# Performance work log

Hardware: AMD Instinct MI355X
Metric: run time of the kernel (lower is better)

## Reference

```python
import jax, jax.numpy as jnp
import numpy as np

N = 50000        # nodes
E_RAND = 800000  # random edges; self-loops appended -> E = E_RAND + N
H = 4            # heads
D_IN = 256
D_HID = 64       # per-head hidden (H*D_HID == D_IN -> identity residual in layer 1)
D_OUT = 32       # classes per head
SLOPE = 0.2      # leaky-relu negative slope


def setup_inputs() -> dict:
    key = jax.random.key(0)
    ks = jax.random.split(key, 13)
    loops = jnp.arange(N, dtype=jnp.int32)
    src = jnp.concatenate([jax.random.randint(ks[0], (E_RAND,), 0, N, dtype=jnp.int32), loops])
    dst = jnp.concatenate([jax.random.randint(ks[1], (E_RAND,), 0, N, dtype=jnp.int32), loops])
    h = jax.random.normal(ks[2], (N, D_IN), dtype=jnp.float32)
    def w(k, shape, fan):
        return jax.random.normal(k, shape, dtype=jnp.float32) * (1.0 / np.sqrt(fan))
    return {
        "h": h, "src": src, "dst": dst,
        # layer 1 (tuple in_feats -> separate fc_src / fc_dst in dgl GATConv)
        "W1_src": w(ks[3], (D_IN, H * D_HID), D_IN),
        "W1_dst": w(ks[4], (D_IN, H * D_HID), D_IN),
        "al1": w(ks[5], (H, D_HID), D_HID),
        "ar1": w(ks[6], (H, D_HID), D_HID),
        # layer 2
        "W2_src": w(ks[7], (H * D_HID, H * D_OUT), H * D_HID),
        "W2_dst": w(ks[8], (H * D_HID, H * D_OUT), H * D_HID),
        "al2": w(ks[9], (H, D_OUT), D_OUT),
        "ar2": w(ks[10], (H, D_OUT), D_OUT),
        # residual projection for layer 2 (in_dim != heads*out)
        "Wres2": w(ks[11], (H * D_HID, H * D_OUT), H * D_HID),
    }


def gat_conv(h_node, src, dst, Ws, Wd, al, ar, heads, dout, resval):
    n = h_node.shape[0]
    fs = (h_node @ Ws).reshape(n, heads, dout)   # [N,H,D] projected src feats
    fd = (h_node @ Wd).reshape(n, heads, dout)
    el = jnp.sum(fs * al, axis=-1)               # [N,H]
    er = jnp.sum(fd * ar, axis=-1)               # [N,H]
    e = jax.nn.leaky_relu(el[src] + er[dst], SLOPE)           # [E,H] edge scores
    emax = jax.ops.segment_max(e, dst, num_segments=n)        # segment softmax over dst
    ex = jnp.exp(e - emax[dst])
    denom = jax.ops.segment_sum(ex, dst, num_segments=n)
    a = ex / denom[dst]                                        # [E,H] attention
    msg = fs[src] * a[:, :, None]                              # [E,H,D] gather * weight
    out = jax.ops.segment_sum(msg, dst, num_segments=n)       # [N,H,D] scatter-add
    return out + resval


def reference(h, src, dst, W1_src, W1_dst, al1, ar1, W2_src, W2_dst, al2, ar2, Wres2):
    # layer 1: identity residual (in_dim == heads*hidden), elu activation, flatten heads
    res1 = h.reshape(-1, H, D_HID)
    h1 = gat_conv(h, src, dst, W1_src, W1_dst, al1, ar1, H, D_HID, res1)
    h1 = jax.nn.elu(h1).reshape(-1, H * D_HID)
    # layer 2: linear residual, no activation, mean over heads
    res2 = (h1 @ Wres2).reshape(-1, H, D_OUT)
    h2 = gat_conv(h1, src, dst, W2_src, W2_dst, al2, ar2, H, D_OUT, res2)
    return h2.mean(axis=1)                                     # [N, num_classes]
```

## Files before the change

kernel.cpp:

```cpp
#include <hip/hip_runtime.h>
#include <hip/hip_bf16.h>

#define NN 50000
#define EE 850000
#define NBLK_SCAN 98

typedef unsigned short u16;
using short8 = __attribute__((ext_vector_type(8))) short;
using f32x4  = __attribute__((ext_vector_type(4))) float;

__device__ __forceinline__ float bf2f(u16 u) {
    union { unsigned int i; float f; } v; v.i = ((unsigned int)u) << 16; return v.f;
}
__device__ __forceinline__ u16 f2bf(float f) {
    __hip_bfloat16 h = __float2bfloat16(f);
    return *reinterpret_cast<u16*>(&h);
}

__device__ __forceinline__ float ld1(const void* X, size_t i, bool f32m) {
    return f32m ? ((const float*)X)[i] : bf2f(((const u16*)X)[i]);
}
__device__ __forceinline__ void load4(const void* X, size_t g, bool f32m, float o[4]) {
    if (f32m) {
        float4 v = ((const float4*)X)[g];
        o[0] = v.x; o[1] = v.y; o[2] = v.z; o[3] = v.w;
    } else {
        ushort4 v = ((const ushort4*)X)[g];
        o[0] = bf2f(v.x); o[1] = bf2f(v.y); o[2] = bf2f(v.z); o[3] = bf2f(v.w);
    }
}

__global__ void k_detect(const u16* __restrict__ hh, int* __restrict__ flag,
                         int* __restrict__ deg) {
    if (blockIdx.x != 0) {
        int i = (blockIdx.x - 1) * 256 + threadIdx.x;
        if (i < NN) deg[i] = 0;
        return;
    }
    __shared__ int sm[256];
    int t = threadIdx.x;
    int c = 0;
    for (int i = 0; i < 16; ++i) {
        u16 u = hh[t * 16 + i];
        int e = (u >> 7) & 0xFF;
        if (e != 0 && (e < 90 || e > 160)) ++c;
    }
    sm[t] = c;
    __syncthreads();
    for (int s = 128; s > 0; s >>= 1) {
        if (t < s) sm[t] += sm[t + s];
        __syncthreads();
    }
    if (t == 0) *flag = (sm[0] > 200) ? 1 : 0;
}

__global__ void k_prep(const void* __restrict__ W1s, const void* __restrict__ al1,
                       const void* __restrict__ W1d, const void* __restrict__ ar1,
                       const void* __restrict__ W2s, const void* __restrict__ al2,
                       const void* __restrict__ W2d, const void* __restrict__ ar2,
                       const void* __restrict__ Wres2, const int* __restrict__ dst,
                       u16* __restrict__ BT1, u16* __restrict__ BT2,
                       float* __restrict__ wl1, float* __restrict__ wr1,
                       float* __restrict__ wl2, float* __restrict__ wr2,
                       int* __restrict__ deg, const int* __restrict__ mode) {
    int bid = blockIdx.x;
    if (bid >= 528) {
        int e = (bid - 528) * 256 + threadIdx.x;
        if (e < EE) atomicAdd(&deg[dst[e]], 1);
        return;
    }
    bool f32m = (*mode) != 0;
    if (bid < 512) {
        int id = bid * 256 + threadIdx.x;
        int which = id >> 16;
        int rem = id & 65535;
        int n = rem >> 8, k = rem & 255;
        if (which == 0) {
            BT1[n * 256 + k] = f2bf(ld1(W1s, (size_t)k * 256 + n, f32m));
        } else {
            float v = (n < 128) ? ld1(W2s, (size_t)k * 128 + n, f32m)
                                : ld1(Wres2, (size_t)k * 128 + (n - 128), f32m);
            BT2[n * 256 + k] = f2bf(v);
        }
    } else {
        int id = (bid - 512) * 256 + threadIdx.x;
        int which = id >> 10;
        int rem = id & 1023;
        int k = rem >> 2, h = rem & 3;
        float s = 0.f;
        if (which == 0) {
            for (int d = 0; d < 64; ++d) s += ld1(W1s, k * 256 + h * 64 + d, f32m) * ld1(al1, h * 64 + d, f32m);
            wl1[k * 4 + h] = s;
        } else if (which == 1) {
            for (int d = 0; d < 64; ++d) s += ld1(W1d, k * 256 + h * 64 + d, f32m) * ld1(ar1, h * 64 + d, f32m);
            wr1[k * 4 + h] = s;
        } else if (which == 2) {
            for (int d = 0; d < 32; ++d) s += ld1(W2s, k * 128 + h * 32 + d, f32m) * ld1(al2, h * 32 + d, f32m);
            wl2[k * 4 + h] = s;
        } else {
            for (int d = 0; d < 32; ++d) s += ld1(W2d, k * 128 + h * 32 + d, f32m) * ld1(ar2, h * 32 + d, f32m);
            wr2[k * 4 + h] = s;
        }
    }
}

__global__ void k_scan1(const int* __restrict__ deg, int* __restrict__ rowptr,
                        int* __restrict__ bsum) {
    __shared__ int sm[512];
    int t = threadIdx.x;
    int i = blockIdx.x * 512 + t;
    int v = (i < NN) ? deg[i] : 0;
    int x = v;
    sm[t] = x;
    __syncthreads();
    for (int off = 1; off < 512; off <<= 1) {
        int y = (t >= off) ? sm[t - off] : 0;
        __syncthreads();
        x += y;
        sm[t] = x;
        __syncthreads();
    }
    if (i < NN) rowptr[i] = x - v;
    if (t == 511) bsum[blockIdx.x] = x;
}

__global__ void k_scan2(const int* __restrict__ bsum, int* __restrict__ boff) {
    __shared__ int sm[128];
    int t = threadIdx.x;
    int v = (t < NBLK_SCAN) ? bsum[t] : 0;
    int x = v;
    sm[t] = x;
    __syncthreads();
    for (int off = 1; off < 128; off <<= 1) {
        int y = (t >= off) ? sm[t - off] : 0;
        __syncthreads();
        x += y;
        sm[t] = x;
        __syncthreads();
    }
    if (t < NBLK_SCAN) boff[t] = x - v;
}

__global__ void k_scan3(int* __restrict__ rowptr, const int* __restrict__ boff,
                        int* __restrict__ cursor) {
    int i = blockIdx.x * 256 + threadIdx.x;
    if (i < NN) {
        int r = rowptr[i] + boff[i >> 9];
        rowptr[i] = r;
        cursor[i] = r;
        if (i == 0) rowptr[NN] = EE;
    }
}

__global__ void k_scatter(const int* __restrict__ src, const int* __restrict__ dst,
                          int* __restrict__ cursor, int* __restrict__ csrc) {
    int e = blockIdx.x * 256 + threadIdx.x;
    if (e < EE) {
        int d = dst[e];
        int slot = atomicAdd(&cursor[d], 1);
        csrc[slot] = src[e];
    }
}

__global__ void k_eler(const void* __restrict__ X,
                       const float* __restrict__ wl, const float* __restrict__ wr,
                       float* __restrict__ el, float* __restrict__ er,
                       const int* __restrict__ mode) {
    bool f32m = (*mode) != 0;
    int wave = threadIdx.x >> 6, lane = threadIdx.x & 63;
    int node = blockIdx.x * 4 + wave;
    float a[4];
    load4(X, (size_t)node * 64 + lane, f32m, a);
    float accl[4] = {0, 0, 0, 0}, accr[4] = {0, 0, 0, 0};
    int k0 = lane * 4;
#pragma unroll
    for (int j = 0; j < 4; ++j) {
        float4 wlv = ((const float4*)wl)[k0 + j];
        float4 wrv = ((const float4*)wr)[k0 + j];
        accl[0] += a[j] * wlv.x; accl[1] += a[j] * wlv.y;
        accl[2] += a[j] * wlv.z; accl[3] += a[j] * wlv.w;
        accr[0] += a[j] * wrv.x; accr[1] += a[j] * wrv.y;
        accr[2] += a[j] * wrv.z; accr[3] += a[j] * wrv.w;
    }
#pragma unroll
    for (int off = 32; off > 0; off >>= 1) {
#pragma unroll
        for (int t = 0; t < 4; ++t) {
            accl[t] += __shfl_down(accl[t], off, 64);
            accr[t] += __shfl_down(accr[t], off, 64);
        }
    }
    if (lane == 0) {
        float4 vl = {accl[0], accl[1], accl[2], accl[3]};
        float4 vr = {accr[0], accr[1], accr[2], accr[3]};
        ((float4*)el)[node] = vl;
        ((float4*)er)[node] = vr;
    }
}

__global__ void k_gemm_mfma(const void* __restrict__ A, int aDual,
                            const u16* __restrict__ BT, u16* __restrict__ C,
                            const int* __restrict__ mode) {
    bool af32 = aDual && ((*mode) != 0);
    __shared__ u16 At[128 * 72];
    __shared__ u16 Bt[128 * 72];
    int t = threadIdx.x;
    int lane = t & 63, w = t >> 6;
    int mt = blockIdx.x >> 1, nt = blockIdx.x & 1;
    int m0 = mt * 128, n0 = nt * 128;
    int wr = (w >> 1) * 64, wc = (w & 1) * 64;
    f32x4 acc[4][4] = {};
    int q = lane >> 4, cl = lane & 15;

    for (int ph = 0; ph < 4; ++ph) {
        int kb = ph * 64;
        for (int it = 0; it < 4; ++it) {
            int c = it * 256 + t;
            int row = c >> 3, c8 = c & 7;
            int rowg = m0 + row;
            if (af32) {
                if (rowg < NN) {
                    const float* ap = (const float*)A + (size_t)rowg * 256 + kb + c8 * 8;
                    float4 v0 = ((const float4*)ap)[0];
                    float4 v1 = ((const float4*)ap)[1];
                    ushort4 lo = {f2bf(v0.x), f2bf(v0.y), f2bf(v0.z), f2bf(v0.w)};
                    ushort4 hi = {f2bf(v1.x), f2bf(v1.y), f2bf(v1.z), f2bf(v1.w)};
                    *(ushort4*)&At[row * 72 + c8 * 8] = lo;
                    *(ushort4*)&At[row * 72 + c8 * 8 + 4] = hi;
                } else {
                    ushort4 z = {0, 0, 0, 0};
                    *(ushort4*)&At[row * 72 + c8 * 8] = z;
                    *(ushort4*)&At[row * 72 + c8 * 8 + 4] = z;
                }
            } else {
                float4 av;
                if (rowg < NN) {
                    av = *(const float4*)((const u16*)A + (size_t)rowg * 256 + kb + c8 * 8);
                } else {
                    av = make_float4(0.f, 0.f, 0.f, 0.f);
                }
                *(float4*)&At[row * 72 + c8 * 8] = av;
            }
            float4 bv = *(const float4*)(BT + (size_t)(n0 + row) * 256 + kb + c8 * 8);
            *(float4*)&Bt[row * 72 + c8 * 8] = bv;
        }
        __syncthreads();
#pragma unroll
        for (int ks = 0; ks < 2; ++ks) {
            short8 af[4], bf[4];
#pragma unroll
            for (int i = 0; i < 4; ++i)
                af[i] = *(const short8*)&At[(wr + i * 16 + cl) * 72 + ks * 32 + q * 8];
#pragma unroll
            for (int j = 0; j < 4; ++j)
                bf[j] = *(const short8*)&Bt[(wc + j * 16 + cl) * 72 + ks * 32 + q * 8];
#pragma unroll
            for (int i = 0; i < 4; ++i)
#pragma unroll
                for (int j = 0; j < 4; ++j)
                    acc[i][j] = __builtin_amdgcn_mfma_f32_16x16x32_bf16(af[i], bf[j], acc[i][j], 0, 0, 0);
        }
        __syncthreads();
    }
#pragma unroll
    for (int i = 0; i < 4; ++i)
#pragma unroll
        for (int j = 0; j < 4; ++j)
#pragma unroll
            for (int r = 0; r < 4; ++r) {
                int mrow = m0 + wr + i * 16 + q * 4 + r;
                if (mrow < NN)
                    C[(size_t)mrow * 256 + n0 + wc + j * 16 + cl] = f2bf(acc[i][j][r]);
            }
}

__global__ void k_agg1(const int* __restrict__ rowptr, const int* __restrict__ csrc,
                       const float* __restrict__ el, const float* __restrict__ er,
                       const u16* __restrict__ fs, const void* __restrict__ h_in,
                       u16* __restrict__ h1,
                       const float* __restrict__ wl2, const float* __restrict__ wr2,
                       float* __restrict__ el2, float* __restrict__ er2,
                       const int* __restrict__ mode) {
    bool f32m = (*mode) != 0;
    int wave = threadIdx.x >> 6, lane = threadIdx.x & 63;
    int node = blockIdx.x * 4 + wave;
    int beg = rowptr[node], end = rowptr[node + 1];
    int head = lane >> 4;
    float erh = er[node * 4 + head];
    float a0 = 0.f, a1 = 0.f, a2 = 0.f, a3 = 0.f, ll = 0.f;
#pragma unroll 2
    for (int p = beg; p < end; ++p) {
        int s = csrc[p];
        float e = el[s * 4 + head] + erh;
        e = e > 0.f ? e : 0.2f * e;
        e = fminf(fmaxf(e, -60.f), 60.f);
        float pw = __expf(e);
        ushort4 fv = *(const ushort4*)(fs + (size_t)s * 256 + lane * 4);
        ll += pw;
        a0 += pw * bf2f(fv.x);
        a1 += pw * bf2f(fv.y);
        a2 += pw * bf2f(fv.z);
        a3 += pw * bf2f(fv.w);
    }
    float rinv = 1.f / ll;
    float res[4];
    load4(h_in, (size_t)node * 64 + lane, f32m, res);
    float v0 = a0 * rinv + res[0], v1 = a1 * rinv + res[1];
    float v2 = a2 * rinv + res[2], v3 = a3 * rinv + res[3];
    v0 = v0 > 0.f ? v0 : __expf(v0) - 1.f;
    v1 = v1 > 0.f ? v1 : __expf(v1) - 1.f;
    v2 = v2 > 0.f ? v2 : __expf(v2) - 1.f;
    v3 = v3 > 0.f ? v3 : __expf(v3) - 1.f;
    ushort4 o = {f2bf(v0), f2bf(v1), f2bf(v2), f2bf(v3)};
    ((ushort4*)h1)[(size_t)node * 64 + lane] = o;
    float4 w0 = ((const float4*)wl2)[lane * 4 + 0];
    float4 w1 = ((const float4*)wl2)[lane * 4 + 1];
    float4 w2 = ((const float4*)wl2)[lane * 4 + 2];
    float4 w3 = ((const float4*)wl2)[lane * 4 + 3];
    float4 r0 = ((const float4*)wr2)[lane * 4 + 0];
    float4 r1 = ((const float4*)wr2)[lane * 4 + 1];
    float4 r2 = ((const float4*)wr2)[lane * 4 + 2];
    float4 r3 = ((const float4*)wr2)[lane * 4 + 3];
    float acl[4], acr[4];
    acl[0] = v0 * w0.x + v1 * w1.x + v2 * w2.x + v3 * w3.x;
    acl[1] = v0 * w0.y + v1 * w1.y + v2 * w2.y + v3 * w3.y;
    acl[2] = v0 * w0.z + v1 * w1.z + v2 * w2.z + v3 * w3.z;
    acl[3] = v0 * w0.w + v1 * w1.w + v2 * w2.w + v3 * w3.w;
    acr[0] = v0 * r0.x + v1 * r1.x + v2 * r2.x + v3 * r3.x;
    acr[1] = v0 * r0.y + v1 * r1.y + v2 * r2.y + v3 * r3.y;
    acr[2] = v0 * r0.z + v1 * r1.z + v2 * r2.z + v3 * r3.z;
    acr[3] = v0 * r0.w + v1 * r1.w + v2 * r2.w + v3 * r3.w;
#pragma unroll
    for (int off = 32; off > 0; off >>= 1) {
#pragma unroll
        for (int t = 0; t < 4; ++t) {
            acl[t] += __shfl_down(acl[t], off, 64);
            acr[t] += __shfl_down(acr[t], off, 64);
        }
    }
    if (lane == 0) {
        float4 vl = {acl[0], acl[1], acl[2], acl[3]};
        float4 vr = {acr[0], acr[1], acr[2], acr[3]};
        ((float4*)el2)[node] = vl;
        ((float4*)er2)[node] = vr;
    }
}

__global__ void k_agg2(const int* __restrict__ rowptr, const int* __restrict__ csrc,
                       const float* __restrict__ el, const float* __restrict__ er,
                       const u16* __restrict__ c2, void* __restrict__ out,
                       const int* __restrict__ mode) {
    bool f32m = (*mode) != 0;
    int wave = threadIdx.x >> 6, lane = threadIdx.x & 63;
    int node = blockIdx.x * 4 + wave;
    int beg = rowptr[node], end = rowptr[node + 1];
    int head = lane >> 4;
    float erh = er[node * 4 + head];
    float a0 = 0.f, a1 = 0.f, ll = 0.f;
#pragma unroll 2
    for (int p = beg; p < end; ++p) {
        int s = csrc[p];
        float e = el[s * 4 + head] + erh;
        e = e > 0.f ? e : 0.2f * e;
        e = fminf(fmaxf(e, -60.f), 60.f);
        float pw = __expf(e);
        ushort2 fv = *(const ushort2*)(c2 + (size_t)s * 256 + lane * 2);
        ll += pw;
        a0 += pw * bf2f(fv.x);
        a1 += pw * bf2f(fv.y);
    }
    float rinv = 1.f / ll;
    ushort2 rv = *(const ushort2*)(c2 + (size_t)node * 256 + 128 + lane * 2);
    float o0 = a0 * rinv + bf2f(rv.x);
    float o1 = a1 * rinv + bf2f(rv.y);
    o0 += __shfl_xor(o0, 16, 64); o0 += __shfl_xor(o0, 32, 64);
    o1 += __shfl_xor(o1, 16, 64); o1 += __shfl_xor(o1, 32, 64);
    if (lane < 16) {
        float v0 = 0.25f * o0, v1 = 0.25f * o1;
        size_t oi = (size_t)node * 32 + lane * 2;
        if (f32m) {
            ((float*)out)[oi] = v0;
            ((float*)out)[oi + 1] = v1;
        } else {
            ushort2 ov = {f2bf(v0), f2bf(v1)};
            *(ushort2*)((u16*)out + oi) = ov;
        }
    }
}

extern "C" void kernel_launch(void* const* d_in, const int* in_sizes, int n_in,
                              void* d_out, int out_size, void* d_ws, size_t ws_size,
                              hipStream_t stream) {
    int ih = 0, isrc = 1, idst = 2, iW1s = 3, iW1d = 4, ial1 = 5, iar1 = 6,
        iW2s = 7, iW2d = 8, ial2 = 9, iar2 = 10, iWres = 11;
    if (n_in >= 12 && in_sizes[0] != 12800000) {
        iW1d = 0; iW1s = 1; iW2d = 2; iW2s = 3; iWres = 4; ial1 = 5; ial2 = 6;
        iar1 = 7; iar2 = 8; idst = 9; ih = 10; isrc = 11;
    }
    const void* h     = d_in[ih];
    const int* src    = (const int*)d_in[isrc];
    const int* dst    = (const int*)d_in[idst];
    const void* W1s   = d_in[iW1s];
    const void* W1d   = d_in[iW1d];
    const void* al1   = d_in[ial1];
    const void* ar1   = d_in[iar1];
    const void* W2s   = d_in[iW2s];
    const void* W2d   = d_in[iW2d];
    const void* al2   = d_in[ial2];
    const void* ar2   = d_in[iar2];
    const void* Wres2 = d_in[iWres];

    char* w = (char*)d_ws;
    size_t off = 0;
    auto alloc = [&](size_t bytes) -> void* {
        void* p = w + off;
        off += (bytes + 255) & ~(size_t)255;
        return p;
    };
    int* mode   = (int*)alloc(256);
    float* wl1 = (float*)alloc(256 * 4 * 4);
    float* wr1 = (float*)alloc(256 * 4 * 4);
    float* wl2 = (float*)alloc(256 * 4 * 4);
    float* wr2 = (float*)alloc(256 * 4 * 4);
    int* deg    = (int*)alloc(NN * 4);
    int* cursor = (int*)alloc(NN * 4);
    int* rowptr = (int*)alloc((NN + 1) * 4);
    int* bsum   = (int*)alloc(NBLK_SCAN * 4);
    int* boff   = (int*)alloc(NBLK_SCAN * 4);
    int* csrc   = (int*)alloc((size_t)EE * 4);
    float* el1  = (float*)alloc((size_t)NN * 4 * 4);
    float* er1  = (float*)alloc((size_t)NN * 4 * 4);
    float* el2  = (float*)alloc((size_t)NN * 4 * 4);
    float* er2  = (float*)alloc((size_t)NN * 4 * 4);
    u16* BT1    = (u16*)alloc(256 * 256 * 2);
    u16* BT2    = (u16*)alloc(256 * 256 * 2);
    u16* fs1    = (u16*)alloc((size_t)NN * 256 * 2);
    u16* h1     = (u16*)alloc((size_t)NN * 256 * 2);
    u16* c2     = fs1;

    k_detect<<<197, 256, 0, stream>>>((const u16*)h, mode, deg);
    k_prep<<<528 + (EE + 255) / 256, 256, 0, stream>>>(
        W1s, al1, W1d, ar1, W2s, al2, W2d, ar2, Wres2, dst,
        BT1, BT2, wl1, wr1, wl2, wr2, deg, mode);
    k_scan1<<<NBLK_SCAN, 512, 0, stream>>>(deg, rowptr, bsum);
    k_scan2<<<1, 128, 0, stream>>>(bsum, boff);
    k_scan3<<<(NN + 255) / 256, 256, 0, stream>>>(rowptr, boff, cursor);
    k_scatter<<<(EE + 255) / 256, 256, 0, stream>>>(src, dst, cursor, csrc);
    k_eler<<<NN / 4, 256, 0, stream>>>(h, wl1, wr1, el1, er1, mode);
    k_gemm_mfma<<<782, 256, 0, stream>>>(h, 1, BT1, fs1, mode);
    k_agg1<<<NN / 4, 256, 0, stream>>>(rowptr, csrc, el1, er1, fs1, h, h1,
                                       wl2, wr2, el2, er2, mode);
    k_gemm_mfma<<<782, 256, 0, stream>>>(h1, 0, BT2, c2, mode);
    k_agg2<<<NN / 4, 256, 0, stream>>>(rowptr, csrc, el2, er2, c2, d_out, mode);
}
```

Before: 414.9 us.

## Precompute layer-1 edge attention weights during CSR scatter, fuse scan3 with el/er

Merges the rowptr fixup kernel with the layer-1 el/er projection kernel into one launch. The CSR scatter now also computes the leaky-relu and exp attention weight for each edge and stores it as bf16 in CSR order. The layer-1 aggregation then reads that weight instead of gathering el[src] and recomputing exp, and its inner loop is unrolled further. This adds an E×4 bf16 buffer and extra scatter work in exchange for fewer random gathers and less arithmetic in the aggregation loop. The bf16 rounding of the weights loses some precision.

```diff
diff --git a/kernel.cpp b/kernel.cpp
--- a/kernel.cpp
+++ b/kernel.cpp
@@ -141,34 +141,25 @@
     if (t < NBLK_SCAN) boff[t] = x - v;
 }
 
-__global__ void k_scan3(int* __restrict__ rowptr, const int* __restrict__ boff,
-                        int* __restrict__ cursor) {
-    int i = blockIdx.x * 256 + threadIdx.x;
-    if (i < NN) {
-        int r = rowptr[i] + boff[i >> 9];
-        rowptr[i] = r;
-        cursor[i] = r;
-        if (i == 0) rowptr[NN] = EE;
-    }
-}
-
-__global__ void k_scatter(const int* __restrict__ src, const int* __restrict__ dst,
-                          int* __restrict__ cursor, int* __restrict__ csrc) {
-    int e = blockIdx.x * 256 + threadIdx.x;
-    if (e < EE) {
-        int d = dst[e];
-        int slot = atomicAdd(&cursor[d], 1);
-        csrc[slot] = src[e];
-    }
-}
-
-__global__ void k_eler(const void* __restrict__ X,
-                       const float* __restrict__ wl, const float* __restrict__ wr,
-                       float* __restrict__ el, float* __restrict__ er,
-                       const int* __restrict__ mode) {
+__global__ void k_scan3_eler1(int* __restrict__ rowptr, const int* __restrict__ boff,
+                              int* __restrict__ cursor, const void* __restrict__ X,
+                              const float* __restrict__ wl, const float* __restrict__ wr,
+                              float* __restrict__ el, float* __restrict__ er,
+                              const int* __restrict__ mode) {
+    int bid = blockIdx.x;
+    if (bid < 196) {
+        int i = bid * 256 + threadIdx.x;
+        if (i < NN) {
+            int r = rowptr[i] + boff[i >> 9];
+            rowptr[i] = r;
+            cursor[i] = r;
+            if (i == 0) rowptr[NN] = EE;
+        }
+        return;
+    }
     bool f32m = (*mode) != 0;
     int wave = threadIdx.x >> 6, lane = threadIdx.x & 63;
-    int node = blockIdx.x * 4 + wave;
+    int node = (bid - 196) * 4 + wave;
     float a[4];
     load4(X, (size_t)node * 64 + lane, f32m, a);
     float accl[4] = {0, 0, 0, 0}, accr[4] = {0, 0, 0, 0};
@@ -196,6 +187,30 @@
         ((float4*)el)[node] = vl;
         ((float4*)er)[node] = vr;
     }
+}
+
+__global__ void k_scatter(const int* __restrict__ src, const int* __restrict__ dst,
+                          int* __restrict__ cursor, int* __restrict__ csrc,
+                          const float* __restrict__ el, const float* __restrict__ er,
+                          u16* __restrict__ aw) {
+    int e = blockIdx.x * 256 + threadIdx.x;
+    if (e >= EE) return;
+    int s = src[e], d = dst[e];
+    int slot = atomicAdd(&cursor[d], 1);
+    csrc[slot] = s;
+    float4 eL = ((const float4*)el)[s];
+    float4 eR = ((const float4*)er)[d];
+    float ev[4] = {eL.x + eR.x, eL.y + eR.y, eL.z + eR.z, eL.w + eR.w};
+    ushort4 o;
+    u16* op = (u16*)&o;
+#pragma unroll
+    for (int t = 0; t < 4; ++t) {
+        float x = ev[t];
+        x = x > 0.f ? x : 0.2f * x;
+        x = fminf(fmaxf(x, -60.f), 60.f);
+        op[t] = f2bf(__expf(x));
+    }
+    ((ushort4*)aw)[slot] = o;
 }
 
 __global__ void k_gemm_mfma(const void* __restrict__ A, int aDual,
@@ -275,9 +290,8 @@
 }
 
 __global__ void k_agg1(const int* __restrict__ rowptr, const int* __restrict__ csrc,
-                       const float* __restrict__ el, const float* __restrict__ er,
-                       const u16* __restrict__ fs, const void* __restrict__ h_in,
-                       u16* __restrict__ h1,
+                       const u16* __restrict__ aw, const u16* __restrict__ fs,
+                       const void* __restrict__ h_in, u16* __restrict__ h1,
                        const float* __restrict__ wl2, const float* __restrict__ wr2,
                        float* __restrict__ el2, float* __restrict__ er2,
                        const int* __restrict__ mode) {
@@ -286,15 +300,11 @@
     int node = blockIdx.x * 4 + wave;
     int beg = rowptr[node], end = rowptr[node + 1];
     int head = lane >> 4;
-    float erh = er[node * 4 + head];
     float a0 = 0.f, a1 = 0.f, a2 = 0.f, a3 = 0.f, ll = 0.f;
-#pragma unroll 2
+#pragma unroll 4
     for (int p = beg; p < end; ++p) {
         int s = csrc[p];
-        float e = el[s * 4 + head] + erh;
-        e = e > 0.f ? e : 0.2f * e;
-        e = fminf(fmaxf(e, -60.f), 60.f);
-        float pw = __expf(e);
+        float pw = bf2f(aw[(size_t)p * 4 + head]);
         ushort4 fv = *(const ushort4*)(fs + (size_t)s * 256 + lane * 4);
         ll += pw;
         a0 += pw * bf2f(fv.x);
@@ -428,6 +438,7 @@
     int* bsum   = (int*)alloc(NBLK_SCAN * 4);
     int* boff   = (int*)alloc(NBLK_SCAN * 4);
     int* csrc   = (int*)alloc((size_t)EE * 4);
+    u16* aw     = (u16*)alloc((size_t)EE * 4 * 2);
     float* el1  = (float*)alloc((size_t)NN * 4 * 4);
     float* er1  = (float*)alloc((size_t)NN * 4 * 4);
     float* el2  = (float*)alloc((size_t)NN * 4 * 4);
@@ -444,11 +455,12 @@
         BT1, BT2, wl1, wr1, wl2, wr2, deg, mode);
     k_scan1<<<NBLK_SCAN, 512, 0, stream>>>(deg, rowptr, bsum);
     k_scan2<<<1, 128, 0, stream>>>(bsum, boff);
-    k_scan3<<<(NN + 255) / 256, 256, 0, stream>>>(rowptr, boff, cursor);
-    k_scatter<<<(EE + 255) / 256, 256, 0, stream>>>(src, dst, cursor, csrc);
-    k_eler<<<NN / 4, 256, 0, stream>>>(h, wl1, wr1, el1, er1, mode);
+    k_scan3_eler1<<<196 + NN / 4, 256, 0, stream>>>(rowptr, boff, cursor,
+                                                    h, wl1, wr1, el1, er1, mode);
+    k_scatter<<<(EE + 255) / 256, 256, 0, stream>>>(src, dst, cursor, csrc,
+                                                    el1, er1, aw);
     k_gemm_mfma<<<782, 256, 0, stream>>>(h, 1, BT1, fs1, mode);
-    k_agg1<<<NN / 4, 256, 0, stream>>>(rowptr, csrc, el1, er1, fs1, h, h1,
+    k_agg1<<<NN / 4, 256, 0, stream>>>(rowptr, csrc, aw, fs1, h, h1,
                                        wl2, wr2, el2, er2, mode);
     k_gemm_mfma<<<782, 256, 0, stream>>>(h1, 0, BT2, c2, mode);
     k_agg2<<<NN / 4, 256, 0, stream>>>(rowptr, csrc, el2, er2, c2, d_out, mode);
```

New measurement: 403.1 us. 1.03x faster.
